# Optimization experiments

Measured on AMD Instinct MI355X. Metric: run time of the kernel, lower is better.

## Reference

```python
import jax, jax.numpy as jnp
import numpy as np

SR = 44100
D = SR * 30          # duration_samples = 1_323_000
N = 1024             # number of note events
L = 32768            # max note length in samples
W = 1024             # hann window length (module's window_length)
H = 8                # harmonics in the synth
K = 128              # FIR taps in the effect chain
LAT = 2              # time_latent_size


def setup_inputs() -> dict:
    key = jax.random.key(0)
    ks = jax.random.split(key, 10)
    freq_rad = jax.random.uniform(ks[0], (N,), jnp.float32, 0.01, 0.3)
    velocity = jax.random.uniform(ks[1], (N,), jnp.float32, 1.0, 127.0)
    starts = jax.random.randint(ks[2], (N,), 0, D - L, dtype=jnp.int32)
    lengths = jax.random.randint(ks[3], (N,), 2048, L + 1, dtype=jnp.int32)
    # time_embedder: Linear(1,32) -> ReLU -> Linear(32,LAT)
    w1 = jax.random.normal(ks[4], (1, 32), jnp.float32)
    b1 = jnp.zeros((32,), jnp.float32)
    w2 = jax.random.normal(ks[5], (32, LAT), jnp.float32) / jnp.sqrt(32.0)
    b2 = jnp.zeros((LAT,), jnp.float32)
    # synth amplitude MLP: [freq, vel, latent] (2+LAT) -> 64 -> H
    ws1 = jax.random.normal(ks[6], (2 + LAT, 64), jnp.float32)
    bs1 = jnp.zeros((64,), jnp.float32)
    ws2 = jax.random.normal(ks[7], (64, H), jnp.float32) / 8.0
    bs2 = jnp.zeros((H,), jnp.float32)
    # effect chain: causal FIR (OIW layout) + tanh
    fir = jax.random.normal(ks[8], (1, 1, K), jnp.float32) / K
    return dict(freq_rad=freq_rad, velocity=velocity,
                w1=w1, b1=b1, w2=w2, b2=b2,
                ws1=ws1, bs1=bs1, ws2=ws2, bs2=bs2, fir=fir,
                starts=starts, lengths=lengths, duration_samples=D)


def reference(freq_rad, velocity, w1, b1, w2, b2, ws1, bs1, ws2, bs2, fir,
              starts, lengths, duration_samples):
    Dn = int(duration_samples)
    t = jnp.arange(L, dtype=jnp.float32)            # [L]
    ti = jnp.arange(L, dtype=jnp.int32)             # [L]
    ends = starts + lengths
    # output_length = min(end, duration) - start, clipped to [0, L]
    out_len = jnp.clip(jnp.minimum(ends, Dn) - starts, 0, L)  # [N]
    # time latent: MLP on normalized start time
    nt = (starts.astype(jnp.float32) / Dn)[:, None]           # [N,1]
    lat = jax.nn.relu(nt @ w1 + b1) @ w2 + b2                  # [N,LAT]
    vel = (velocity / 127.0)[:, None]                          # [N,1]
    # harmonic amplitudes from tiny MLP (the 'synth')
    feat = jnp.concatenate([freq_rad[:, None], vel, lat], axis=-1)  # [N,2+LAT]
    amps = jax.nn.softplus(jax.nn.relu(feat @ ws1 + bs1) @ ws2 + bs2)  # [N,H]
    # additive synthesis; fixed small loop over harmonics, vectorized over [N,L]
    phase = freq_rad[:, None] * t[None, :]                     # [N,L]
    seg = jnp.zeros((N, L), jnp.float32)
    for hh in range(1, H + 1):
        seg = seg + amps[:, hh - 1:hh] * jnp.sin(hh * phase)
    seg = seg * vel
    # hann window (torch periodic) on the LAST W samples of each variable-length segment
    n = jnp.arange(W, dtype=jnp.float32)
    hann = 0.5 * (1.0 - jnp.cos(2.0 * jnp.pi * n / W))         # [W]
    wpos = ti[None, :] - (out_len[:, None] - W)                # [N,L]
    in_win = (wpos >= 0) & (wpos < W)
    factor = jnp.where(in_win, hann[jnp.clip(wpos, 0, W - 1)], 1.0)
    mask = (ti[None, :] < out_len[:, None]).astype(jnp.float32)  # zero past segment end
    seg = seg * factor * mask
    # effect chain: causal 128-tap FIR then tanh (masked so padding stays silent)
    y = jax.lax.conv_general_dilated(seg[:, None, :], fir,
                                     window_strides=(1,), padding=[(K - 1, 0)])
    seg = jnp.tanh(y[:, 0, :]) * mask                          # [N,L]
    # overlap-add: scatter each note into the output buffer
    idx = starts[:, None] + ti[None, :]                        # [N,L]
    valid = (ti[None, :] < out_len[:, None]) & (idx < Dn)
    contrib = jnp.where(valid, seg, 0.0)
    out = jnp.zeros((Dn,), jnp.float32).at[jnp.clip(idx, 0, Dn - 1).reshape(-1)].add(
        contrib.reshape(-1))
    return out
```

## Files before the change

### kernel.cpp

```cpp
#include <hip/hip_runtime.h>
#include <math.h>

#define LMAX  32768
#define WWIN  1024
#define KFIR  128
#define WOUT  512
#define TO    1024
#define CPAD  656
#define NMAX  1024
#define PMAX  96

typedef _Float16 v8h __attribute__((ext_vector_type(8)));
typedef _Float16 v4h __attribute__((ext_vector_type(4)));
typedef float    v4f __attribute__((ext_vector_type(4)));

__device__ __forceinline__ float fast_tanh(float x) {
    float e = __builtin_amdgcn_exp2f(x * 2.8853900817779268f);
    return fmaf(-2.0f, __builtin_amdgcn_rcpf(e + 1.0f), 1.0f);
}

__global__ __launch_bounds__(128, 3) void synth_fused_k(
    const float* __restrict__ freq_g, const float* __restrict__ velo_g,
    const float* __restrict__ w1,  const float* __restrict__ b1,
    const float* __restrict__ w2,  const float* __restrict__ b2,
    const float* __restrict__ ws1, const float* __restrict__ bs1,
    const float* __restrict__ ws2, const float* __restrict__ bs2,
    const float* __restrict__ fir,
    const int* __restrict__ starts, const int* __restrict__ lengths,
    float* __restrict__ out, int Dn, int N)
{
    __shared__ __align__(16) _Float16 segc[2][4][CPAD];
    __shared__ float fir_s[KFIR];
    __shared__ unsigned short note_list[NMAX];
    __shared__ int note_cnt;
    __shared__ float s_w1[32], s_b1[32], s_w2[64], s_b2[2];
    __shared__ float s_ws1[256], s_bs1[64], s_ws2[512], s_bs2[8];
    __shared__ int   stl[PMAX], oll[PMAX];
    __shared__ float fl[PMAX];
    __shared__ __align__(16) float ampsl[PMAX][8];

    const int tid  = threadIdx.x;
    const int wid  = tid >> 6;
    const int lane = tid & 63;
    const int m    = lane & 15;
    const int quad = lane >> 4;
    const int o0   = blockIdx.x * TO;
    const int o_end = min(o0 + TO, Dn);
    const int ow   = o0 + wid * WOUT;

    fir_s[tid] = fir[tid];
    if (tid < 32) { s_w1[tid] = w1[tid]; s_b1[tid] = b1[tid]; }
    if (tid < 64) { s_w2[tid] = w2[tid]; s_bs1[tid] = bs1[tid]; }
    if (tid < 2)  s_b2[tid] = b2[tid];
    if (tid < 8)  s_bs2[tid] = bs2[tid];
    s_ws1[tid] = ws1[tid];       s_ws1[tid + 128] = ws1[tid + 128];
    s_ws2[tid] = ws2[tid];       s_ws2[tid + 128] = ws2[tid + 128];
    s_ws2[tid + 256] = ws2[tid + 256]; s_ws2[tid + 384] = ws2[tid + 384];
    if (tid == 0) note_cnt = 0;
    __syncthreads();

    for (int j = tid; j < N; j += 128) {
        int st = starts[j];
        int len = lengths[j];
        int ol = min(st + len, Dn) - st;
        ol = max(0, min(ol, LMAX));
        if (st < o_end && st + ol > o0) {
            int p = atomicAdd(&note_cnt, 1);
            note_list[p] = (unsigned short)j;
        }
    }
    __syncthreads();
    const int K = note_cnt;

    const int kn0 = min(K, PMAX);
    if (tid < kn0) {
        const int nid = (int)note_list[tid];
        int st  = starts[nid];
        int len = lengths[nid];
        int ol  = min(st + len, Dn) - st;
        ol = max(0, min(ol, LMAX));
        stl[tid] = st;
        oll[tid] = ol;
        float v = velo_g[nid] * (1.0f / 127.0f);
        float f = freq_g[nid];
        fl[tid] = f;
        float nt = (float)st / (float)Dn;
        float lat0 = s_b2[0], lat1 = s_b2[1];
        #pragma unroll
        for (int j = 0; j < 32; ++j) {
            float h = fmaxf(fmaf(nt, s_w1[j], s_b1[j]), 0.0f);
            lat0 = fmaf(h, s_w2[j * 2 + 0], lat0);
            lat1 = fmaf(h, s_w2[j * 2 + 1], lat1);
        }
        float acc[8];
        #pragma unroll
        for (int h = 0; h < 8; ++h) acc[h] = s_bs2[h];
        #pragma unroll
        for (int j = 0; j < 64; ++j) {
            float a = s_bs1[j];
            a = fmaf(f,    s_ws1[0 * 64 + j], a);
            a = fmaf(v,    s_ws1[1 * 64 + j], a);
            a = fmaf(lat0, s_ws1[2 * 64 + j], a);
            a = fmaf(lat1, s_ws1[3 * 64 + j], a);
            a = fmaxf(a, 0.0f);
            #pragma unroll
            for (int h = 0; h < 8; ++h)
                acc[h] = fmaf(a, s_ws2[j * 8 + h], acc[h]);
        }
        #pragma unroll
        for (int h = 0; h < 8; ++h) {
            float a = acc[h];
            float sp = fmaxf(a, 0.0f) + log1pf(expf(-fabsf(a)));
            ampsl[tid][h] = sp * v;
        }
    }

    v8h afrag[12];
    #pragma unroll
    for (int t = 0; t < 12; ++t) {
        v8h af;
        #pragma unroll
        for (int j = 0; j < 8; ++j) {
            int idx = 32 * t + 8 * quad + j - 16 * m;
            float fv = (idx >= 0 && idx < KFIR) ? fir_s[idx] : 0.0f;
            af[j] = (_Float16)fv;
        }
        afrag[t] = af;
    }
    for (int z = lane; z < 4 * 20; z += 64) {
        int S = z / 20, off = z % 20;
        segc[wid][S][636 + off] = (_Float16)0.0f;
    }
    __syncthreads();

    const _Float16* __restrict__ bbase = &segc[wid][m & 3][(m & ~3) + 8 * quad];

    float accA0 = 0.f, accA1 = 0.f, accA2 = 0.f, accA3 = 0.f;
    float accB0 = 0.f, accB1 = 0.f, accB2 = 0.f, accB3 = 0.f;

    const double inv2pi = 0.15915494309189535;

    for (int c = 0; c < K; c += PMAX) {
        const int kn = min(K - c, PMAX);

        if (c > 0) {
            __syncthreads();
            if (tid < kn) {
                const int nid = (int)note_list[c + tid];
                int st  = starts[nid];
                int len = lengths[nid];
                int ol  = min(st + len, Dn) - st;
                ol = max(0, min(ol, LMAX));
                stl[tid] = st;
                oll[tid] = ol;
                float v = velo_g[nid] * (1.0f / 127.0f);
                float f = freq_g[nid];
                fl[tid] = f;
                float nt = (float)st / (float)Dn;
                float lat0 = s_b2[0], lat1 = s_b2[1];
                #pragma unroll
                for (int j = 0; j < 32; ++j) {
                    float h = fmaxf(fmaf(nt, s_w1[j], s_b1[j]), 0.0f);
                    lat0 = fmaf(h, s_w2[j * 2 + 0], lat0);
                    lat1 = fmaf(h, s_w2[j * 2 + 1], lat1);
                }
                float acc[8];
                #pragma unroll
                for (int h = 0; h < 8; ++h) acc[h] = s_bs2[h];
                #pragma unroll
                for (int j = 0; j < 64; ++j) {
                    float a = s_bs1[j];
                    a = fmaf(f,    s_ws1[0 * 64 + j], a);
                    a = fmaf(v,    s_ws1[1 * 64 + j], a);
                    a = fmaf(lat0, s_ws1[2 * 64 + j], a);
                    a = fmaf(lat1, s_ws1[3 * 64 + j], a);
                    a = fmaxf(a, 0.0f);
                    #pragma unroll
                    for (int h = 0; h < 8; ++h)
                        acc[h] = fmaf(a, s_ws2[j * 8 + h], acc[h]);
                }
                #pragma unroll
                for (int h = 0; h < 8; ++h) {
                    float a = acc[h];
                    float sp = fmaxf(a, 0.0f) + log1pf(expf(-fabsf(a)));
                    ampsl[tid][h] = sp * v;
                }
            }
            __syncthreads();
        }

        int stN = 0, olN = 0; float fN = 0.f;
        float4 amN0 = {}, amN1 = {};
        if (kn > 0) {
            stN = stl[0]; olN = oll[0]; fN = fl[0];
            amN0 = *(const float4*)&ampsl[0][0];
            amN1 = *(const float4*)&ampsl[0][4];
        }

        for (int kk = 0; kk < kn; ++kk) {
            const int st = stN, ol = olN;
            const float f = fN;
            const float4 am0 = amN0, am1 = amN1;
            if (kk + 1 < kn) {
                stN = stl[kk + 1]; olN = oll[kk + 1]; fN = fl[kk + 1];
                amN0 = *(const float4*)&ampsl[kk + 1][0];
                amN1 = *(const float4*)&ampsl[kk + 1][4];
            }

            const int base = ow - st;
            if (base >= ol || base + WOUT <= 0) continue;

            const float A0 = am0.x, A1 = am0.y, A2 = am0.z, A3 = am0.w;
            const float A4 = am1.x, A5 = am1.y, A6 = am1.z, A7 = am1.w;
            const double fd = (double)f;

            const int tseed = base - 127 + lane;
            double rev0 = fd * (double)tseed * inv2pi;
            float r0 = (float)(rev0 - floor(rev0));
            float s = __builtin_amdgcn_sinf(r0);
            float cc = __builtin_amdgcn_cosf(r0);
            double d64 = fd * 64.0 * inv2pi;
            float r64 = (float)(d64 - floor(d64));
            const float sd = __builtin_amdgcn_sinf(r64);
            const float cd = __builtin_amdgcn_cosf(r64);
            const int wbase = ol - WWIN;

            const bool interior = (base >= 127) && (base + 513 <= wbase);

            if (interior) {
                #pragma unroll
                for (int i = 0; i < 10; ++i) {
                    float tc = cc + cc;
                    float sA = s;
                    float sum = A0 * sA;
                    float sB = tc * sA;              sum = fmaf(A1, sB, sum);
                    float sC = fmaf(tc, sB, -sA);    sum = fmaf(A2, sC, sum);
                    float sD = fmaf(tc, sC, -sB);    sum = fmaf(A3, sD, sum);
                    float sE = fmaf(tc, sD, -sC);    sum = fmaf(A4, sE, sum);
                    float sF = fmaf(tc, sE, -sD);    sum = fmaf(A5, sF, sum);
                    float sG = fmaf(tc, sF, -sE);    sum = fmaf(A6, sG, sum);
                    float sH = fmaf(tc, sG, -sF);    sum = fmaf(A7, sH, sum);
                    _Float16 h = (_Float16)sum;
                    const int x = lane + 64 * i;
                    if (i == 0) {
                        #pragma unroll
                        for (int S = 0; S < 4; ++S)
                            if (x >= S) segc[wid][S][x - S] = h;
                    } else {
                        #pragma unroll
                        for (int S = 0; S < 4; ++S)
                            segc[wid][S][x - S] = h;
                    }
                    float ns = fmaf(s, cd, cc * sd);
                    float nc = fmaf(cc, cd, -(s * sd));
                    s = ns; cc = nc;
                }
            } else {
                #pragma unroll
                for (int i = 0; i < 10; ++i) {
                    int t = tseed + 64 * i;
                    float val = 0.0f;
                    if (t >= 0 && t < ol) {
                        float tc = cc + cc;
                        float sA = s;
                        float sum = A0 * sA;
                        float sB = tc * sA;              sum = fmaf(A1, sB, sum);
                        float sC = fmaf(tc, sB, -sA);    sum = fmaf(A2, sC, sum);
                        float sD = fmaf(tc, sC, -sB);    sum = fmaf(A3, sD, sum);
                        float sE = fmaf(tc, sD, -sC);    sum = fmaf(A4, sE, sum);
                        float sF = fmaf(tc, sE, -sD);    sum = fmaf(A5, sF, sum);
                        float sG = fmaf(tc, sF, -sE);    sum = fmaf(A6, sG, sum);
                        float sH = fmaf(tc, sG, -sF);    sum = fmaf(A7, sH, sum);
                        int wpos = t - wbase;
                        float factor = 1.0f;
                        if (wpos >= 0)
                            factor = 0.5f - 0.5f * __builtin_amdgcn_cosf((float)wpos * (1.0f / WWIN));
                        val = sum * factor;
                    }
                    _Float16 h = (_Float16)val;
                    const int x = lane + 64 * i;
                    if (i == 0) {
                        #pragma unroll
                        for (int S = 0; S < 4; ++S)
                            if (x >= S) segc[wid][S][x - S] = h;
                    } else {
                        #pragma unroll
                        for (int S = 0; S < 4; ++S)
                            segc[wid][S][x - S] = h;
                    }
                    float ns = fmaf(s, cd, cc * sd);
                    float nc = fmaf(cc, cd, -(s * sd));
                    s = ns; cc = nc;
                }
            }

            v4f CA0 = {0.f, 0.f, 0.f, 0.f};
            v4f CA1 = {0.f, 0.f, 0.f, 0.f};
            v4f CB0 = {0.f, 0.f, 0.f, 0.f};
            v4f CB1 = {0.f, 0.f, 0.f, 0.f};
            #pragma unroll
            for (int t = 0; t < 6; ++t) {
                v4h lo = *(const v4h*)(bbase + 32 * t);
                v4h hi = *(const v4h*)(bbase + 32 * t + 4);
                v8h bf = __builtin_shufflevector(lo, hi, 0, 1, 2, 3, 4, 5, 6, 7);
                CA0 = __builtin_amdgcn_mfma_f32_16x16x32_f16(afrag[t], bf, CA0, 0, 0, 0);
                v4h lo2 = *(const v4h*)(bbase + 256 + 32 * t);
                v4h hi2 = *(const v4h*)(bbase + 256 + 32 * t + 4);
                v8h bf2 = __builtin_shufflevector(lo2, hi2, 0, 1, 2, 3, 4, 5, 6, 7);
                CB0 = __builtin_amdgcn_mfma_f32_16x16x32_f16(afrag[t], bf2, CB0, 0, 0, 0);
            }
            #pragma unroll
            for (int t = 6; t < 12; ++t) {
                v4h lo = *(const v4h*)(bbase + 32 * t);
                v4h hi = *(const v4h*)(bbase + 32 * t + 4);
                v8h bf = __builtin_shufflevector(lo, hi, 0, 1, 2, 3, 4, 5, 6, 7);
                CA1 = __builtin_amdgcn_mfma_f32_16x16x32_f16(afrag[t], bf, CA1, 0, 0, 0);
                v4h lo2 = *(const v4h*)(bbase + 256 + 32 * t);
                v4h hi2 = *(const v4h*)(bbase + 256 + 32 * t + 4);
                v8h bf2 = __builtin_shufflevector(lo2, hi2, 0, 1, 2, 3, 4, 5, 6, 7);
                CB1 = __builtin_amdgcn_mfma_f32_16x16x32_f16(afrag[t], bf2, CB1, 0, 0, 0);
            }

            {
                const int tb = base + 64 * quad + m;
                float y;
                y = CA0[0] + CA1[0]; if (tb +   0 >= 0 && tb +   0 < ol) accA0 += fast_tanh(y);
                y = CA0[1] + CA1[1]; if (tb +  16 >= 0 && tb +  16 < ol) accA1 += fast_tanh(y);
                y = CA0[2] + CA1[2]; if (tb +  32 >= 0 && tb +  32 < ol) accA2 += fast_tanh(y);
                y = CA0[3] + CA1[3]; if (tb +  48 >= 0 && tb +  48 < ol) accA3 += fast_tanh(y);
                y = CB0[0] + CB1[0]; if (tb + 256 >= 0 && tb + 256 < ol) accB0 += fast_tanh(y);
                y = CB0[1] + CB1[1]; if (tb + 272 >= 0 && tb + 272 < ol) accB1 += fast_tanh(y);
                y = CB0[2] + CB1[2]; if (tb + 288 >= 0 && tb + 288 < ol) accB2 += fast_tanh(y);
                y = CB0[3] + CB1[3]; if (tb + 304 >= 0 && tb + 304 < ol) accB3 += fast_tanh(y);
            }
        }
    }

    const int ob = ow + 64 * quad + m;
    if (ob +   0 < Dn) out[ob +   0] = accA0;
    if (ob +  16 < Dn) out[ob +  16] = accA1;
    if (ob +  32 < Dn) out[ob +  32] = accA2;
    if (ob +  48 < Dn) out[ob +  48] = accA3;
    if (ob + 256 < Dn) out[ob + 256] = accB0;
    if (ob + 272 < Dn) out[ob + 272] = accB1;
    if (ob + 288 < Dn) out[ob + 288] = accB2;
    if (ob + 304 < Dn) out[ob + 304] = accB3;
}

extern "C" void kernel_launch(void* const* d_in, const int* in_sizes, int n_in,
                              void* d_out, int out_size, void* d_ws, size_t ws_size,
                              hipStream_t stream) {
    const float* freq    = (const float*)d_in[0];
    const float* velo    = (const float*)d_in[1];
    const float* w1      = (const float*)d_in[2];
    const float* b1      = (const float*)d_in[3];
    const float* w2      = (const float*)d_in[4];
    const float* b2      = (const float*)d_in[5];
    const float* ws1     = (const float*)d_in[6];
    const float* bs1     = (const float*)d_in[7];
    const float* ws2     = (const float*)d_in[8];
    const float* bs2     = (const float*)d_in[9];
    const float* fir     = (const float*)d_in[10];
    const int*   starts  = (const int*)d_in[11];
    const int*   lengths = (const int*)d_in[12];

    const int N  = in_sizes[0];
    const int Dn = out_size;
    float* out = (float*)d_out;

    int n_tiles = (Dn + TO - 1) / TO;
    synth_fused_k<<<n_tiles, 128, 0, stream>>>(
        freq, velo, w1, b1, w2, b2, ws1, bs1, ws2, bs2,
        fir, starts, lengths, out, Dn, N);
}
```

Before: 141.5 us.

## Split note loop across two wave groups per tile with LDS reduction

Measured after the change: 209.0 us. 47.7% more time.

```diff
diff --git a/kernel.cpp b/kernel.cpp
--- a/kernel.cpp
+++ b/kernel.cpp
@@ -19,7 +19,7 @@
     return fmaf(-2.0f, __builtin_amdgcn_rcpf(e + 1.0f), 1.0f);
 }
 
-__global__ __launch_bounds__(128, 3) void synth_fused_k(
+__global__ __launch_bounds__(256, 4) void synth_fused_k(
     const float* __restrict__ freq_g, const float* __restrict__ velo_g,
     const float* __restrict__ w1,  const float* __restrict__ b1,
     const float* __restrict__ w2,  const float* __restrict__ b2,
@@ -29,7 +29,7 @@
     const int* __restrict__ starts, const int* __restrict__ lengths,
     float* __restrict__ out, int Dn, int N)
 {
-    __shared__ __align__(16) _Float16 segc[2][4][CPAD];
+    __shared__ __align__(16) _Float16 segc[4][4][CPAD];
     __shared__ float fir_s[KFIR];
     __shared__ unsigned short note_list[NMAX];
     __shared__ int note_cnt;
@@ -44,22 +44,22 @@
     const int lane = tid & 63;
     const int m    = lane & 15;
     const int quad = lane >> 4;
+    const int grp  = wid >> 1;
     const int o0   = blockIdx.x * TO;
     const int o_end = min(o0 + TO, Dn);
-    const int ow   = o0 + wid * WOUT;
-
-    fir_s[tid] = fir[tid];
+    const int ow   = o0 + (wid & 1) * WOUT;
+
+    if (tid < 128) fir_s[tid] = fir[tid];
     if (tid < 32) { s_w1[tid] = w1[tid]; s_b1[tid] = b1[tid]; }
     if (tid < 64) { s_w2[tid] = w2[tid]; s_bs1[tid] = bs1[tid]; }
     if (tid < 2)  s_b2[tid] = b2[tid];
     if (tid < 8)  s_bs2[tid] = bs2[tid];
-    s_ws1[tid] = ws1[tid];       s_ws1[tid + 128] = ws1[tid + 128];
-    s_ws2[tid] = ws2[tid];       s_ws2[tid + 128] = ws2[tid + 128];
-    s_ws2[tid + 256] = ws2[tid + 256]; s_ws2[tid + 384] = ws2[tid + 384];
+    s_ws1[tid] = ws1[tid];
+    s_ws2[tid] = ws2[tid];  s_ws2[tid + 256] = ws2[tid + 256];
     if (tid == 0) note_cnt = 0;
     __syncthreads();
 
-    for (int j = tid; j < N; j += 128) {
+    for (int j = tid; j < N; j += 256) {
         int st = starts[j];
         int len = lengths[j];
         int ol = min(st + len, Dn) - st;
@@ -191,20 +191,20 @@
 
         int stN = 0, olN = 0; float fN = 0.f;
         float4 amN0 = {}, amN1 = {};
-        if (kn > 0) {
-            stN = stl[0]; olN = oll[0]; fN = fl[0];
-            amN0 = *(const float4*)&ampsl[0][0];
-            amN1 = *(const float4*)&ampsl[0][4];
-        }
-
-        for (int kk = 0; kk < kn; ++kk) {
+        if (grp < kn) {
+            stN = stl[grp]; olN = oll[grp]; fN = fl[grp];
+            amN0 = *(const float4*)&ampsl[grp][0];
+            amN1 = *(const float4*)&ampsl[grp][4];
+        }
+
+        for (int kk = grp; kk < kn; kk += 2) {
             const int st = stN, ol = olN;
             const float f = fN;
             const float4 am0 = amN0, am1 = amN1;
-            if (kk + 1 < kn) {
-                stN = stl[kk + 1]; olN = oll[kk + 1]; fN = fl[kk + 1];
-                amN0 = *(const float4*)&ampsl[kk + 1][0];
-                amN1 = *(const float4*)&ampsl[kk + 1][4];
+            if (kk + 2 < kn) {
+                stN = stl[kk + 2]; olN = oll[kk + 2]; fN = fl[kk + 2];
+                amN0 = *(const float4*)&ampsl[kk + 2][0];
+                amN1 = *(const float4*)&ampsl[kk + 2][4];
             }
 
             const int base = ow - st;
@@ -336,15 +336,31 @@
         }
     }
 
-    const int ob = ow + 64 * quad + m;
-    if (ob +   0 < Dn) out[ob +   0] = accA0;
-    if (ob +  16 < Dn) out[ob +  16] = accA1;
-    if (ob +  32 < Dn) out[ob +  32] = accA2;
-    if (ob +  48 < Dn) out[ob +  48] = accA3;
-    if (ob + 256 < Dn) out[ob + 256] = accB0;
-    if (ob + 272 < Dn) out[ob + 272] = accB1;
-    if (ob + 288 < Dn) out[ob + 288] = accB2;
-    if (ob + 304 < Dn) out[ob + 304] = accB3;
+    __syncthreads();
+    float* red = (float*)&segc[0][0][0];
+    const int rb = (wid & 1) * WOUT + 64 * quad + m;
+    if (grp == 1) {
+        red[rb +   0] = accA0;
+        red[rb +  16] = accA1;
+        red[rb +  32] = accA2;
+        red[rb +  48] = accA3;
+        red[rb + 256] = accB0;
+        red[rb + 272] = accB1;
+        red[rb + 288] = accB2;
+        red[rb + 304] = accB3;
+    }
+    __syncthreads();
+    if (grp == 0) {
+        const int ob = o0 + rb;
+        if (ob +   0 < Dn) out[ob +   0] = accA0 + red[rb +   0];
+        if (ob +  16 < Dn) out[ob +  16] = accA1 + red[rb +  16];
+        if (ob +  32 < Dn) out[ob +  32] = accA2 + red[rb +  32];
+        if (ob +  48 < Dn) out[ob +  48] = accA3 + red[rb +  48];
+        if (ob + 256 < Dn) out[ob + 256] = accB0 + red[rb + 256];
+        if (ob + 272 < Dn) out[ob + 272] = accB1 + red[rb + 272];
+        if (ob + 288 < Dn) out[ob + 288] = accB2 + red[rb + 288];
+        if (ob + 304 < Dn) out[ob + 304] = accB3 + red[rb + 304];
+    }
 }
 
 extern "C" void kernel_launch(void* const* d_in, const int* in_sizes, int n_in,
@@ -369,7 +385,7 @@
     float* out = (float*)d_out;
 
     int n_tiles = (Dn + TO - 1) / TO;
-    synth_fused_k<<<n_tiles, 128, 0, stream>>>(
+    synth_fused_k<<<n_tiles, 256, 0, stream>>>(
         freq, velo, w1, b1, w2, b2, ws1, bs1, ws2, bs2,
         fir, starts, lengths, out, Dn, N);
 }
```
